# Optimization experiments

Measured on AMD Instinct MI355X. Metric: run time of the kernel, lower is better.

## Reference

```python
import jax, jax.numpy as jnp
import numpy as np

B, L, C = 8, 8192, 256
FOCAL_LEVEL = 3
KERNELS = [3, 5, 7]  # focal_factor*k + focal_x[0]
LN_EPS = 1e-3  # keras LayerNormalization default epsilon


def _gelu(x):
    return jax.nn.gelu(x, approximate=False)  # keras 'gelu' is exact


def _layernorm(x, g, b):
    m = jnp.mean(x, axis=-1, keepdims=True)
    v = jnp.var(x, axis=-1, keepdims=True)
    return (x - m) * jax.lax.rsqrt(v + LN_EPS) * g + b


def _conv1d_same(x, w, b):
    # x: [B,L,Cin], w: [K,Cin,Cout]
    y = jax.lax.conv_general_dilated(x, w, window_strides=(1,), padding='SAME',
                                     dimension_numbers=('NWC', 'WIO', 'NWC'))
    return y + b


def setup_inputs() -> dict:
    key = jax.random.key(0)
    ks = jax.random.split(key, 16)
    s = 0.02
    inp = {
        'x': jax.random.normal(ks[0], (B, L, C), dtype=jnp.float32),
        'f_w': jax.random.normal(ks[1], (C, 2 * C + FOCAL_LEVEL + 1), dtype=jnp.float32) * s,
        'f_b': jnp.zeros((2 * C + FOCAL_LEVEL + 1,), dtype=jnp.float32),
        'h_w': jax.random.normal(ks[2], (1, C, C), dtype=jnp.float32) * s,
        'h_b': jnp.zeros((C,), dtype=jnp.float32),
        'proj_w': jax.random.normal(ks[3], (C, C), dtype=jnp.float32) * s,
        'proj_b': jnp.zeros((C,), dtype=jnp.float32),
    }
    for l, K in enumerate(KERNELS):
        inp[f'conv_w{l}'] = jax.random.normal(ks[4 + l], (K, C, C), dtype=jnp.float32) * s
        inp[f'conv_b{l}'] = jnp.zeros((C,), dtype=jnp.float32)
        inp[f'ln_g{l}'] = jnp.ones((C,), dtype=jnp.float32)
        inp[f'ln_b{l}'] = jnp.zeros((C,), dtype=jnp.float32)
    return inp


def reference(x, f_w, f_b,
              conv_w0, conv_b0, ln_g0, ln_b0,
              conv_w1, conv_b1, ln_g1, ln_b1,
              conv_w2, conv_b2, ln_g2, ln_b2,
              h_w, h_b, proj_w, proj_b):
    x_fea = x @ f_w + f_b                      # [B,L,2C+4]
    q = x_fea[..., :C]
    ctx = x_fea[..., C:2 * C]
    gates = x_fea[..., 2 * C:]                 # [B,L,4]

    levels = [(conv_w0, conv_b0, ln_g0, ln_b0),
              (conv_w1, conv_b1, ln_g1, ln_b1),
              (conv_w2, conv_b2, ln_g2, ln_b2)]

    ctx_all = jnp.zeros_like(ctx)
    for l, (cw, cb, lg, lb) in enumerate(levels):
        ctx = _layernorm(_gelu(_conv1d_same(ctx, cw, cb)), lg, lb)
        ctx_all = ctx_all + ctx * gates[..., l:l + 1]

    # global average pool gate (broadcasts over L)
    ctx_global = jnp.mean(ctx, axis=1, keepdims=True) * gates[..., FOCAL_LEVEL:]
    ctx_all = ctx_all + ctx_global

    # h: 1x1 conv == dense
    ctx_all = jnp.einsum('blc,cd->bld', ctx_all, h_w[0]) + h_b
    x_out = (q * ctx_all) @ proj_w + proj_b    # proj_drop is identity at inference
    return x_out
```

## Files before the change

kernel.cpp:

```cpp
#include <hip/hip_runtime.h>
#include <math.h>

#define CDIM 256
#define LSEQ 8192
#define BATCH 8
#define MTOT (BATCH * LSEQ)
#define PADROWS 8208
#define PAD0 8

typedef unsigned short ushort_t;
typedef unsigned int uint_t;

typedef __bf16 bf16x8 __attribute__((ext_vector_type(8)));
typedef float f32x4 __attribute__((ext_vector_type(4)));

__device__ __forceinline__ ushort_t f2bf(float f) {
    union { float f; uint_t u; } v; v.f = f;
    uint_t u = v.u;
    return (ushort_t)((u + 0x7FFFu + ((u >> 16) & 1u)) >> 16);
}
__device__ __forceinline__ float bf2f(ushort_t h) {
    union { uint_t u; float f; } v; v.u = ((uint_t)h) << 16;
    return v.f;
}
__device__ __forceinline__ float gelu_exact(float x) {
    return 0.5f * x * (1.0f + erff(x * 0.70710678118654752440f));
}

__device__ __forceinline__ void gload16(const ushort_t* g, ushort_t* lds) {
    __builtin_amdgcn_global_load_lds(
        reinterpret_cast<__attribute__((address_space(1))) uint_t*>(
            reinterpret_cast<uintptr_t>(g)),
        reinterpret_cast<__attribute__((address_space(3))) uint_t*>(
            reinterpret_cast<uintptr_t>(lds)),
        16, 0, 0);
}

__global__ __launch_bounds__(256) void cvt_f32_bf16(const float* __restrict__ in,
                                                    ushort_t* __restrict__ out) {
    int i = blockIdx.x * 256 + threadIdx.x;
    float4 v = ((const float4*)in)[i];
    ushort4 o = { f2bf(v.x), f2bf(v.y), f2bf(v.z), f2bf(v.w) };
    ((ushort4*)out)[i] = o;
}

__global__ __launch_bounds__(256) void transpose_cvt(const float* __restrict__ in,
                                                     ushort_t* __restrict__ out,
                                                     int K, int N, int ldin, int col0) {
    __shared__ float t[32][33];
    int k0 = blockIdx.x * 32, n0 = blockIdx.y * 32;
    int tx = threadIdx.x, ty = threadIdx.y;
    #pragma unroll
    for (int i = 0; i < 4; i++) {
        int k = k0 + ty + i * 8;
        t[ty + i * 8][tx] = in[(size_t)k * ldin + col0 + n0 + tx];
    }
    __syncthreads();
    #pragma unroll
    for (int i = 0; i < 4; i++) {
        int n = n0 + ty + i * 8;
        out[(size_t)n * K + k0 + tx] = f2bf(t[tx][ty + i * 8]);
    }
}

__global__ __launch_bounds__(256) void zero_guards(ushort_t* __restrict__ ctx_pad) {
    int i = blockIdx.x * 256 + threadIdx.x;
    int c = i & 255;
    int r = (i >> 8) & 15;
    int b = i >> 12;
    int row = b * PADROWS + ((r < 8) ? r : (PADROWS - 16 + r));
    ctx_pad[(size_t)row * CDIM + c] = 0;
}

template <int MODE>
__global__ __launch_bounds__(256) void gemm_bf16(
    const ushort_t* __restrict__ A, const ushort_t* __restrict__ BT,
    const float* __restrict__ bias,
    float* __restrict__ C, ushort_t* __restrict__ q_out, ushort_t* __restrict__ ctx_pad,
    int Ktot)
{
    __shared__ __align__(16) ushort_t As[128 * 32];
    __shared__ __align__(16) ushort_t Bs[128 * 32];
    int tid = threadIdx.x;
    int w = tid >> 6, l = tid & 63;
    int bn = blockIdx.x * 128;
    int by = blockIdx.y;
    long arow0 = (long)by * 128;
    int crow0 = by * 128;

    int wr = w >> 1, wc = w & 1;
    int lr = l & 15, lk = (l >> 4) * 8;
    int sr = l >> 2;
    int sc = (l & 3) * 8;

    f32x4 acc[4][4] = {};

    int nsteps = Ktot >> 5;
    for (int kt = 0; kt < nsteps; ++kt) {
        int k0 = kt << 5;
        #pragma unroll
        for (int jj = 0; jj < 2; ++jj) {
            int j = w * 2 + jj;
            int r = j * 16 + sr;
            gload16(A + (arow0 + r) * CDIM + (k0 + sc), &As[j * 512]);
            gload16(BT + (long)(bn + r) * Ktot + (k0 + sc), &Bs[j * 512]);
        }
        __syncthreads();
        bf16x8 av[4], bv[4];
        #pragma unroll
        for (int m = 0; m < 4; ++m)
            av[m] = *reinterpret_cast<const bf16x8*>(&As[(wr * 64 + m * 16 + lr) * 32 + lk]);
        #pragma unroll
        for (int n = 0; n < 4; ++n)
            bv[n] = *reinterpret_cast<const bf16x8*>(&Bs[(wc * 64 + n * 16 + lr) * 32 + lk]);
        #pragma unroll
        for (int m = 0; m < 4; ++m)
            #pragma unroll
            for (int n = 0; n < 4; ++n)
                acc[m][n] = __builtin_amdgcn_mfma_f32_16x16x32_bf16(av[m], bv[n], acc[m][n], 0, 0, 0);
        __syncthreads();
    }

    int rbase = (l >> 4) * 4;
    #pragma unroll
    for (int n = 0; n < 4; ++n) {
        int col = bn + wc * 64 + n * 16 + lr;
        float bia = bias[col];
        #pragma unroll
        for (int m = 0; m < 4; ++m) {
            int rowb = crow0 + wr * 64 + m * 16 + rbase;
            #pragma unroll
            for (int r = 0; r < 4; ++r) {
                float v = acc[m][n][r] + bia;
                int row = rowb + r;
                if (MODE == 0) {
                    C[(size_t)row * CDIM + col] = v;
                } else if (MODE == 1) {
                    if (col < CDIM) {
                        q_out[(size_t)row * CDIM + col] = f2bf(v);
                    } else {
                        int bb = row >> 13, tb = row & (LSEQ - 1);
                        ctx_pad[((size_t)bb * PADROWS + PAD0 + tb) * CDIM + (col - CDIM)] = f2bf(v);
                    }
                } else {
                    size_t idx = (size_t)row * CDIM + col;
                    q_out[idx] = f2bf(bf2f(q_out[idx]) * v);
                }
            }
        }
    }
}

__global__ __launch_bounds__(512) void conv_fused(
    const ushort_t* __restrict__ A, const ushort_t* __restrict__ BT,
    const float* __restrict__ bias,
    const float* __restrict__ lng, const float* __restrict__ lnb,
    ushort_t* __restrict__ ctx_out, int KW, int Ktot)
{
    __shared__ __align__(16) ushort_t As[144 * 256];
    __shared__ __align__(16) ushort_t Bs[2][256 * 32];
    __shared__ float rs[128][4], rq[128][4];

    int tid = threadIdx.x;
    int w = tid >> 6, l = tid & 63;
    int by = blockIdx.x;
    int b = by >> 6;
    int tloc = (by & 63) << 7;
    const ushort_t* Arow0 = A + ((size_t)b * PADROWS + PAD0 + tloc - 8) * CDIM;

    int wr = w >> 2;
    int wc = w & 3;
    int lr = l & 15, lk = (l >> 4) * 8;
    int quad = l >> 4;

    #pragma unroll
    for (int i = 0; i < 9; ++i) {
        int o = tid + i * 512;
        int row = o >> 5, cp = o & 31;
        int cg = cp ^ (row & 7);
        gload16(Arow0 + (size_t)row * CDIM + cg * 8, &As[(w * 64 + i * 512) * 8]);
    }
    {
        #pragma unroll
        for (int i = 0; i < 2; ++i) {
            int o = tid + i * 512;
            int n = o >> 2, cp = o & 3;
            int cg = cp ^ ((n >> 1) & 3);
            gload16(BT + (size_t)n * Ktot + cg * 8, &Bs[0][(w * 64 + i * 512) * 8]);
        }
    }
    __syncthreads();

    int P = KW >> 1;
    int hoff = 8 - P;
    f32x4 acc[4][4] = {};
    int nIt = KW * 8;

    for (int it = 0; it < nIt; ++it) {
        int nx = it + 1;
        if (nx < nIt) {
            int tapn = nx >> 3, c0n = nx & 7;
            #pragma unroll
            for (int i = 0; i < 2; ++i) {
                int o = tid + i * 512;
                int n = o >> 2, cp = o & 3;
                int cg = cp ^ ((n >> 1) & 3);
                gload16(BT + (size_t)n * Ktot + (tapn * 256 + c0n * 32 + cg * 8),
                        &Bs[nx & 1][(w * 64 + i * 512) * 8]);
            }
        }
        int tap = it >> 3, c0 = it & 7;
        int buf = it & 1;
        bf16x8 av[4], bv[4];
        #pragma unroll
        for (int m = 0; m < 4; ++m) {
            int row = wr * 64 + m * 16 + lr + tap + hoff;
            int C = c0 * 4 + (lk >> 3);
            int cs = (C & ~7) | ((C ^ row) & 7);
            av[m] = *reinterpret_cast<const bf16x8*>(&As[row * 256 + cs * 8]);
        }
        #pragma unroll
        for (int n = 0; n < 4; ++n) {
            int nn = wc * 64 + n * 16 + lr;
            int cs = (lk >> 3) ^ ((nn >> 1) & 3);
            bv[n] = *reinterpret_cast<const bf16x8*>(&Bs[buf][nn * 32 + cs * 8]);
        }
        #pragma unroll
        for (int m = 0; m < 4; ++m)
            #pragma unroll
            for (int n = 0; n < 4; ++n)
                acc[m][n] = __builtin_amdgcn_mfma_f32_16x16x32_bf16(av[m], bv[n], acc[m][n], 0, 0, 0);
        __syncthreads();
    }

    float bias_c[4], lng_c[4], lnb_c[4];
    #pragma unroll
    for (int n = 0; n < 4; ++n) {
        int col = wc * 64 + n * 16 + lr;
        bias_c[n] = bias[col];
        lng_c[n] = lng[col];
        lnb_c[n] = lnb[col];
    }
    #pragma unroll
    for (int m = 0; m < 4; ++m) {
        #pragma unroll
        for (int r = 0; r < 4; ++r) {
            float s = 0.0f, sq = 0.0f;
            #pragma unroll
            for (int n = 0; n < 4; ++n) {
                float v = acc[m][n][r] + bias_c[n];
                v = gelu_exact(v);
                acc[m][n][r] = v;
                s += v; sq += v * v;
            }
            s += __shfl_xor(s, 1);  sq += __shfl_xor(sq, 1);
            s += __shfl_xor(s, 2);  sq += __shfl_xor(sq, 2);
            s += __shfl_xor(s, 4);  sq += __shfl_xor(sq, 4);
            s += __shfl_xor(s, 8);  sq += __shfl_xor(sq, 8);
            if (lr == 0) {
                int rl = wr * 64 + m * 16 + quad * 4 + r;
                rs[rl][wc] = s;
                rq[rl][wc] = sq;
            }
        }
    }
    __syncthreads();
    #pragma unroll
    for (int m = 0; m < 4; ++m) {
        #pragma unroll
        for (int r = 0; r < 4; ++r) {
            int rl = wr * 64 + m * 16 + quad * 4 + r;
            float mean = (rs[rl][0] + rs[rl][1] + rs[rl][2] + rs[rl][3]) * (1.0f / 256.0f);
            float var = (rq[rl][0] + rq[rl][1] + rq[rl][2] + rq[rl][3]) * (1.0f / 256.0f) - mean * mean;
            float inv = rsqrtf(var + 1e-3f);
            int trow = tloc + rl;
            ushort_t* cp = ctx_out + ((size_t)b * PADROWS + PAD0 + trow) * CDIM;
            #pragma unroll
            for (int n = 0; n < 4; ++n) {
                int col = wc * 64 + n * 16 + lr;
                float y = (acc[m][n][r] - mean) * inv * lng_c[n] + lnb_c[n];
                cp[col] = f2bf(y);
            }
        }
    }
}

__global__ __launch_bounds__(256) void gates_kernel(const float* __restrict__ x,
                                                    const float* __restrict__ f_w,
                                                    const float* __restrict__ f_b,
                                                    float* __restrict__ gates) {
    __shared__ float fcol[256][4];
    int tid = threadIdx.x;
    #pragma unroll
    for (int j = 0; j < 4; ++j) fcol[tid][j] = f_w[(size_t)tid * 516 + 512 + j];
    __syncthreads();
    int w = tid >> 6, l = tid & 63;
    int t = blockIdx.x * 4 + w;
    float4 xv = ((const float4*)(x + (size_t)t * CDIM))[l];
    int c = l * 4;
    float a[4];
    #pragma unroll
    for (int j = 0; j < 4; ++j)
        a[j] = xv.x * fcol[c][j] + xv.y * fcol[c + 1][j] + xv.z * fcol[c + 2][j] + xv.w * fcol[c + 3][j];
    #pragma unroll
    for (int off = 32; off >= 1; off >>= 1)
        #pragma unroll
        for (int j = 0; j < 4; ++j) a[j] += __shfl_xor(a[j], off);
    if (l == 0) {
        #pragma unroll
        for (int j = 0; j < 4; ++j) gates[(size_t)t * 4 + j] = a[j] + f_b[512 + j];
    }
}

__global__ __launch_bounds__(256) void col_mean_partial(const ushort_t* __restrict__ ctx_pad,
                                                        float* __restrict__ partial) {
    int b = blockIdx.x, chunk = blockIdx.y, c = threadIdx.x;
    const ushort_t* base = ctx_pad + ((size_t)b * PADROWS + PAD0 + chunk * 256) * CDIM + c;
    float s = 0.0f;
    for (int r = 0; r < 256; ++r) s += bf2f(base[(size_t)r * CDIM]);
    partial[((size_t)b * 32 + chunk) * CDIM + c] = s;
}

__global__ __launch_bounds__(256) void col_mean_final(const float* __restrict__ partial,
                                                      float* __restrict__ meanv) {
    int b = blockIdx.x, c = threadIdx.x;
    float s = 0.0f;
    for (int i = 0; i < 32; ++i) s += partial[((size_t)b * 32 + i) * CDIM + c];
    meanv[b * CDIM + c] = s * (1.0f / (float)LSEQ);
}

__global__ __launch_bounds__(256) void finalize_A(
    const ushort_t* __restrict__ c0buf, const ushort_t* __restrict__ c1buf,
    const ushort_t* __restrict__ c2buf,
    const float* __restrict__ meanv, const float* __restrict__ gates,
    ushort_t* __restrict__ A_bf)
{
    int i = blockIdx.x * 256 + threadIdx.x;
    int t = i >> 5;
    int c8 = (i & 31) * 8;
    int b = t >> 13, tb = t & (LSEQ - 1);
    size_t pidx = ((size_t)b * PADROWS + PAD0 + tb) * CDIM + c8;
    const float* g = gates + (size_t)t * 4;
    float g0 = g[0], g1 = g[1], g2 = g[2], g3 = g[3];
    ushort4 a0 = *(const ushort4*)(c0buf + pidx);
    ushort4 a1 = *(const ushort4*)(c0buf + pidx + 4);
    ushort4 b0 = *(const ushort4*)(c1buf + pidx);
    ushort4 b1 = *(const ushort4*)(c1buf + pidx + 4);
    ushort4 d0 = *(const ushort4*)(c2buf + pidx);
    ushort4 d1 = *(const ushort4*)(c2buf + pidx + 4);
    const float* mv = meanv + b * CDIM + c8;
    ushort_t out[8];
    ushort_t va[8] = { a0.x, a0.y, a0.z, a0.w, a1.x, a1.y, a1.z, a1.w };
    ushort_t vb[8] = { b0.x, b0.y, b0.z, b0.w, b1.x, b1.y, b1.z, b1.w };
    ushort_t vd[8] = { d0.x, d0.y, d0.z, d0.w, d1.x, d1.y, d1.z, d1.w };
    #pragma unroll
    for (int j = 0; j < 8; ++j) {
        float v = bf2f(va[j]) * g0 + bf2f(vb[j]) * g1 + bf2f(vd[j]) * g2 + mv[j] * g3;
        out[j] = f2bf(v);
    }
    *(ushort4*)(A_bf + (size_t)t * CDIM + c8)     = make_ushort4(out[0], out[1], out[2], out[3]);
    *(ushort4*)(A_bf + (size_t)t * CDIM + c8 + 4) = make_ushort4(out[4], out[5], out[6], out[7]);
}

extern "C" void kernel_launch(void* const* d_in, const int* in_sizes, int n_in,
                              void* d_out, int out_size, void* d_ws, size_t ws_size,
                              hipStream_t stream) {
    const float* x      = (const float*)d_in[0];
    const float* f_w    = (const float*)d_in[1];
    const float* f_b    = (const float*)d_in[2];
    const float* h_w    = (const float*)d_in[3];
    const float* h_b    = (const float*)d_in[4];
    const float* proj_w = (const float*)d_in[5];
    const float* proj_b = (const float*)d_in[6];
    const float* conv_w[3] = { (const float*)d_in[7],  (const float*)d_in[11], (const float*)d_in[15] };
    const float* conv_b[3] = { (const float*)d_in[8],  (const float*)d_in[12], (const float*)d_in[16] };
    const float* ln_g[3]   = { (const float*)d_in[9],  (const float*)d_in[13], (const float*)d_in[17] };
    const float* ln_b[3]   = { (const float*)d_in[10], (const float*)d_in[14], (const float*)d_in[18] };

    const size_t MC = (size_t)MTOT * CDIM;
    const size_t PADC = (size_t)BATCH * PADROWS * CDIM;
    char* w = (char*)d_ws;
    ushort_t* x_bf  = (ushort_t*)w;  w += MC * 2;
    ushort_t* q_bf  = (ushort_t*)w;  w += MC * 2;
    ushort_t* ctxF  = (ushort_t*)w;  w += PADC * 2;
    ushort_t* ctx0  = (ushort_t*)w;  w += PADC * 2;
    ushort_t* ctx1  = (ushort_t*)w;  w += PADC * 2;
    ushort_t* ctx2  = (ushort_t*)w;  w += PADC * 2;
    float* gates    = (float*)w;     w += (size_t)MTOT * 4 * 4;
    float* partial  = (float*)w;     w += (size_t)8 * 32 * CDIM * 4;
    float* meanv    = (float*)w;     w += (size_t)8 * CDIM * 4;
    ushort_t* f_wT  = (ushort_t*)w;  w += (size_t)512 * 256 * 2;
    ushort_t* convT0 = (ushort_t*)w; w += (size_t)768 * 256 * 2;
    ushort_t* convT1 = (ushort_t*)w; w += (size_t)1280 * 256 * 2;
    ushort_t* convT2 = (ushort_t*)w; w += (size_t)1792 * 256 * 2;
    ushort_t* h_wT   = (ushort_t*)w; w += (size_t)256 * 256 * 2;
    ushort_t* proj_wT = (ushort_t*)w; w += (size_t)256 * 256 * 2;
    ushort_t* A_bf = x_bf;

    dim3 blk(256);
    dim3 t8(32, 8);

    cvt_f32_bf16<<<dim3(MC / 4 / 256), blk, 0, stream>>>(x, x_bf);
    transpose_cvt<<<dim3(8, 16), t8, 0, stream>>>(f_w, f_wT, 256, 512, 516, 0);
    transpose_cvt<<<dim3(24, 8), t8, 0, stream>>>(conv_w[0], convT0, 768, 256, 256, 0);
    transpose_cvt<<<dim3(40, 8), t8, 0, stream>>>(conv_w[1], convT1, 1280, 256, 256, 0);
    transpose_cvt<<<dim3(56, 8), t8, 0, stream>>>(conv_w[2], convT2, 1792, 256, 256, 0);
    transpose_cvt<<<dim3(8, 8), t8, 0, stream>>>(h_w, h_wT, 256, 256, 256, 0);
    transpose_cvt<<<dim3(8, 8), t8, 0, stream>>>(proj_w, proj_wT, 256, 256, 256, 0);
    zero_guards<<<dim3(128), blk, 0, stream>>>(ctxF);
    zero_guards<<<dim3(128), blk, 0, stream>>>(ctx0);
    zero_guards<<<dim3(128), blk, 0, stream>>>(ctx1);
    zero_guards<<<dim3(128), blk, 0, stream>>>(ctx2);

    gemm_bf16<1><<<dim3(4, 512), blk, 0, stream>>>(x_bf, f_wT, f_b,
        nullptr, q_bf, ctxF, 256);
    gates_kernel<<<dim3(MTOT / 4), blk, 0, stream>>>(x, f_w, f_b, gates);

    conv_fused<<<dim3(512), dim3(512), 0, stream>>>(ctxF, convT0, conv_b[0],
        ln_g[0], ln_b[0], ctx0, 3, 768);
    conv_fused<<<dim3(512), dim3(512), 0, stream>>>(ctx0, convT1, conv_b[1],
        ln_g[1], ln_b[1], ctx1, 5, 1280);
    conv_fused<<<dim3(512), dim3(512), 0, stream>>>(ctx1, convT2, conv_b[2],
        ln_g[2], ln_b[2], ctx2, 7, 1792);

    col_mean_partial<<<dim3(BATCH, 32), blk, 0, stream>>>(ctx2, partial);
    col_mean_final<<<dim3(BATCH), blk, 0, stream>>>(partial, meanv);

    finalize_A<<<dim3(MTOT * 32 / 256), blk, 0, stream>>>(ctx0, ctx1, ctx2,
        meanv, gates, A_bf);

    gemm_bf16<2><<<dim3(2, 512), blk, 0, stream>>>(A_bf, h_wT, h_b,
        nullptr, q_bf, nullptr, 256);
    gemm_bf16<0><<<dim3(2, 512), blk, 0, stream>>>(q_bf, proj_wT, proj_b,
        (float*)d_out, nullptr, nullptr, 256);
}
```

Baseline: 448.1 us.

## Stream conv A tile in 32-channel chunks to shrink LDS and raise occupancy

The conv kernel no longer stages the full 144x256 input halo in shared memory up front. It now double-buffers 32-channel slices of it and reorders the loop to channel-chunk outer, tap inner, with the LayerNorm reduction scratch aliased onto the B buffer. This cuts LDS from about 106KB to about 50KB, and launch bounds now ask for 4 blocks per CU so more blocks can be resident and hide load latency. The cost is extra sync points and a serialized A prefetch at each chunk boundary, and the occupancy hint may force register spilling.

After: 376.9 us. -15.9%, faster.

```diff
diff --git a/kernel.cpp b/kernel.cpp
--- a/kernel.cpp
+++ b/kernel.cpp
@@ -151,15 +151,38 @@
     }
 }
 
-__global__ __launch_bounds__(512) void conv_fused(
+__device__ __forceinline__ void stageA_chunk(const ushort_t* Arow0, int cc,
+                                             ushort_t* asb, int tid, int w) {
+    int o = tid;
+    int row = o >> 2, cp = o & 3;
+    int cg = cp ^ (row & 3);
+    gload16(Arow0 + (size_t)row * CDIM + cc * 32 + cg * 8, asb + (size_t)(w * 64) * 8);
+    if (tid < 64) {
+        int o2 = 512 + tid;
+        int row2 = o2 >> 2, cp2 = o2 & 3;
+        int cg2 = cp2 ^ (row2 & 3);
+        gload16(Arow0 + (size_t)row2 * CDIM + cc * 32 + cg2 * 8, asb + (size_t)512 * 8);
+    }
+}
+__device__ __forceinline__ void stageB_chunk(const ushort_t* BT, int Ktot, int koffB,
+                                             ushort_t* bsb, int tid, int w) {
+    #pragma unroll
+    for (int i = 0; i < 2; ++i) {
+        int o = tid + i * 512;
+        int n = o >> 2, cp = o & 3;
+        int cg = cp ^ ((n >> 1) & 3);
+        gload16(BT + (size_t)n * Ktot + koffB + cg * 8, bsb + (size_t)(w * 64 + i * 512) * 8);
+    }
+}
+
+__global__ __launch_bounds__(512, 4) void conv_fused(
     const ushort_t* __restrict__ A, const ushort_t* __restrict__ BT,
     const float* __restrict__ bias,
     const float* __restrict__ lng, const float* __restrict__ lnb,
     ushort_t* __restrict__ ctx_out, int KW, int Ktot)
 {
-    __shared__ __align__(16) ushort_t As[144 * 256];
+    __shared__ __align__(16) ushort_t As2[2][144 * 32];
     __shared__ __align__(16) ushort_t Bs[2][256 * 32];
-    __shared__ float rs[128][4], rq[128][4];
 
     int tid = threadIdx.x;
     int w = tid >> 6, l = tid & 63;
@@ -170,69 +193,54 @@
 
     int wr = w >> 2;
     int wc = w & 3;
-    int lr = l & 15, lk = (l >> 4) * 8;
+    int lr = l & 15;
     int quad = l >> 4;
-
-    #pragma unroll
-    for (int i = 0; i < 9; ++i) {
-        int o = tid + i * 512;
-        int row = o >> 5, cp = o & 31;
-        int cg = cp ^ (row & 7);
-        gload16(Arow0 + (size_t)row * CDIM + cg * 8, &As[(w * 64 + i * 512) * 8]);
-    }
-    {
-        #pragma unroll
-        for (int i = 0; i < 2; ++i) {
-            int o = tid + i * 512;
-            int n = o >> 2, cp = o & 3;
-            int cg = cp ^ ((n >> 1) & 3);
-            gload16(BT + (size_t)n * Ktot + cg * 8, &Bs[0][(w * 64 + i * 512) * 8]);
-        }
-    }
-    __syncthreads();
 
     int P = KW >> 1;
     int hoff = 8 - P;
     f32x4 acc[4][4] = {};
+
+    stageA_chunk(Arow0, 0, As2[0], tid, w);
+    stageB_chunk(BT, Ktot, 0, Bs[0], tid, w);
+    __syncthreads();
+
     int nIt = KW * 8;
-
-    for (int it = 0; it < nIt; ++it) {
-        int nx = it + 1;
-        if (nx < nIt) {
-            int tapn = nx >> 3, c0n = nx & 7;
-            #pragma unroll
-            for (int i = 0; i < 2; ++i) {
-                int o = tid + i * 512;
-                int n = o >> 2, cp = o & 3;
-                int cg = cp ^ ((n >> 1) & 3);
-                gload16(BT + (size_t)n * Ktot + (tapn * 256 + c0n * 32 + cg * 8),
-                        &Bs[nx & 1][(w * 64 + i * 512) * 8]);
-            }
+    int it = 0;
+    for (int c = 0; c < 8; ++c) {
+        for (int tap = 0; tap < KW; ++tap, ++it) {
+            if (tap == 0 && c < 7)
+                stageA_chunk(Arow0, c + 1, As2[(c + 1) & 1], tid, w);
+            if (it + 1 < nIt) {
+                int tapn = tap + 1, cn = c;
+                if (tapn == KW) { tapn = 0; cn = c + 1; }
+                stageB_chunk(BT, Ktot, tapn * 256 + cn * 32, Bs[(it + 1) & 1], tid, w);
+            }
+            const ushort_t* asb = As2[c & 1];
+            const ushort_t* bsb = Bs[it & 1];
+            bf16x8 av[4], bv[4];
+            #pragma unroll
+            for (int m = 0; m < 4; ++m) {
+                int row = wr * 64 + m * 16 + lr + tap + hoff;
+                int cs = quad ^ (row & 3);
+                av[m] = *reinterpret_cast<const bf16x8*>(&asb[row * 32 + cs * 8]);
+            }
+            #pragma unroll
+            for (int n = 0; n < 4; ++n) {
+                int nn = wc * 64 + n * 16 + lr;
+                int cs = quad ^ ((nn >> 1) & 3);
+                bv[n] = *reinterpret_cast<const bf16x8*>(&bsb[nn * 32 + cs * 8]);
+            }
+            #pragma unroll
+            for (int m = 0; m < 4; ++m)
+                #pragma unroll
+                for (int n = 0; n < 4; ++n)
+                    acc[m][n] = __builtin_amdgcn_mfma_f32_16x16x32_bf16(av[m], bv[n], acc[m][n], 0, 0, 0);
+            __syncthreads();
         }
-        int tap = it >> 3, c0 = it & 7;
-        int buf = it & 1;
-        bf16x8 av[4], bv[4];
-        #pragma unroll
-        for (int m = 0; m < 4; ++m) {
-            int row = wr * 64 + m * 16 + lr + tap + hoff;
-            int C = c0 * 4 + (lk >> 3);
-            int cs = (C & ~7) | ((C ^ row) & 7);
-            av[m] = *reinterpret_cast<const bf16x8*>(&As[row * 256 + cs * 8]);
-        }
-        #pragma unroll
-        for (int n = 0; n < 4; ++n) {
-            int nn = wc * 64 + n * 16 + lr;
-            int cs = (lk >> 3) ^ ((nn >> 1) & 3);
-            bv[n] = *reinterpret_cast<const bf16x8*>(&Bs[buf][nn * 32 + cs * 8]);
-        }
-        #pragma unroll
-        for (int m = 0; m < 4; ++m)
-            #pragma unroll
-            for (int n = 0; n < 4; ++n)
-                acc[m][n] = __builtin_amdgcn_mfma_f32_16x16x32_bf16(av[m], bv[n], acc[m][n], 0, 0, 0);
-        __syncthreads();
-    }
-
+    }
+
+    float* rs = (float*)&Bs[0][0];
+    float* rq = rs + 512;
     float bias_c[4], lng_c[4], lnb_c[4];
     #pragma unroll
     for (int n = 0; n < 4; ++n) {
@@ -259,8 +267,8 @@
             s += __shfl_xor(s, 8);  sq += __shfl_xor(sq, 8);
             if (lr == 0) {
                 int rl = wr * 64 + m * 16 + quad * 4 + r;
-                rs[rl][wc] = s;
-                rq[rl][wc] = sq;
+                rs[rl * 4 + wc] = s;
+                rq[rl * 4 + wc] = sq;
             }
         }
     }
@@ -270,8 +278,8 @@
         #pragma unroll
         for (int r = 0; r < 4; ++r) {
             int rl = wr * 64 + m * 16 + quad * 4 + r;
-            float mean = (rs[rl][0] + rs[rl][1] + rs[rl][2] + rs[rl][3]) * (1.0f / 256.0f);
-            float var = (rq[rl][0] + rq[rl][1] + rq[rl][2] + rq[rl][3]) * (1.0f / 256.0f) - mean * mean;
+            float mean = (rs[rl * 4] + rs[rl * 4 + 1] + rs[rl * 4 + 2] + rs[rl * 4 + 3]) * (1.0f / 256.0f);
+            float var = (rq[rl * 4] + rq[rl * 4 + 1] + rq[rl * 4 + 2] + rq[rl * 4 + 3]) * (1.0f / 256.0f) - mean * mean;
             float inv = rsqrtf(var + 1e-3f);
             int trow = tloc + rl;
             ushort_t* cp = ctx_out + ((size_t)b * PADROWS + PAD0 + trow) * CDIM;
```
